# Kernel optimization log

Measured on AMD Instinct MI355X. Metric: run time of the kernel, lower is better.

## Reference

```python
import jax, jax.numpy as jnp
import numpy as np

B, IN, OUT, GD, TD, H, W, L = 16, 512, 256, 256, 256, 32, 32, 32
EPS_BN = 1e-5


def _conv2d(x, w, pad):
    return jax.lax.conv_general_dilated(
        x, w, window_strides=(1, 1), padding=[(pad, pad), (pad, pad)],
        dimension_numbers=("NCHW", "OIHW", "NCHW"))


def _up2(x):
    return jnp.repeat(jnp.repeat(x, 2, axis=2), 2, axis=3)


def _l2n(v):  # F.normalize(p=2, dim=1), eps=1e-12
    n = jnp.sqrt(jnp.sum(v * v, axis=1, keepdims=True))
    return v / jnp.maximum(n, 1e-12)


def _context(img_embs, words_embs, mask):
    i = _l2n(img_embs)            # [B, TD, P]
    wd = _l2n(words_embs)         # [B, TD, L]
    sim = jnp.einsum("bcp,bcl->bpl", i, wd)
    sim = jnp.where(mask[:, None, :], -jnp.inf, sim)
    attn = jax.nn.softmax(sim, axis=-1)
    return jnp.einsum("bpl,bcl->bcp", attn, wd)  # [B, TD, P]


def _bn(x, w, b):  # training-mode BatchNorm2d, biased variance
    m = jnp.mean(x, axis=(0, 2, 3), keepdims=True)
    v = jnp.var(x, axis=(0, 2, 3), keepdims=True)
    return (x - m) * jax.lax.rsqrt(v + EPS_BN) * w[None, :, None, None] + b[None, :, None, None]


def setup_inputs():
    key = jax.random.key(0)
    ks = jax.random.split(key, 16)
    s = 0.02
    COND = GD + TD
    return {
        "x": jax.random.normal(ks[0], (B, IN, H, W), jnp.float32),
        "global_cond": jax.random.normal(ks[1], (B, GD), jnp.float32),
        "words_embs": jax.random.normal(ks[2], (B, TD, L), jnp.float32),
        "mask": jax.random.randint(ks[3], (B, L), 0, 2).astype(bool),
        "w_img1": jax.random.normal(ks[4], (TD, IN), jnp.float32) * s,
        "w_img2": jax.random.normal(ks[5], (TD, OUT), jnp.float32) * s,
        "w_c1": jax.random.normal(ks[6], (OUT, IN, 3, 3), jnp.float32) * s,
        "w_c2": jax.random.normal(ks[7], (OUT, OUT, 3, 3), jnp.float32) * s,
        "bn1_w": jnp.ones((IN,), jnp.float32),
        "bn1_b": jnp.zeros((IN,), jnp.float32),
        "bn2_w": jnp.ones((OUT,), jnp.float32),
        "bn2_b": jnp.zeros((OUT,), jnp.float32),
        "w_g1": jax.random.normal(ks[8], (IN, COND), jnp.float32) * s,
        "b_g1": jnp.zeros((IN,), jnp.float32),
        "w_b1": jax.random.normal(ks[9], (IN, COND), jnp.float32) * s,
        "b_b1": jnp.zeros((IN,), jnp.float32),
        "w_g2": jax.random.normal(ks[10], (OUT, COND), jnp.float32) * s,
        "b_g2": jnp.zeros((OUT,), jnp.float32),
        "w_b2": jax.random.normal(ks[11], (OUT, COND), jnp.float32) * s,
        "b_b2": jnp.zeros((OUT,), jnp.float32),
        "w_sc": jax.random.normal(ks[12], (OUT, IN, 1, 1), jnp.float32) * s,
        "b_sc": jnp.zeros((OUT,), jnp.float32),
    }


def reference(x, global_cond, words_embs, mask,
              w_img1, w_img2, w_c1, w_c2,
              bn1_w, bn1_b, bn2_w, bn2_b,
              w_g1, b_g1, w_b1, b_b1,
              w_g2, b_g2, w_b2, b_b2,
              w_sc, b_sc):
    # ---- residual path, stage 1 ----
    img1 = jnp.einsum("tc,bcp->btp", w_img1, x.reshape(B, IN, H * W))
    ctx1 = _context(img1, words_embs, mask)                 # [B, TD, H*W]
    gc = jnp.broadcast_to(global_cond[:, :, None], (B, GD, H * W))
    cond1 = jnp.concatenate([gc, ctx1], axis=1)             # [B, GD+TD, H*W]
    gamma1 = jnp.einsum("oc,bcp->bop", w_g1, cond1) + b_g1[None, :, None]
    beta1 = jnp.einsum("oc,bcp->bop", w_b1, cond1) + b_b1[None, :, None]
    out = gamma1.reshape(B, IN, H, W) * _bn(x, bn1_w, bn1_b) + beta1.reshape(B, IN, H, W)
    out = jax.nn.relu(out)
    out = _up2(out)                                         # [B, IN, 2H, 2W]
    out = _conv2d(out, w_c1, 1)                             # [B, OUT, 2H, 2W]
    h2, w2 = 2 * H, 2 * W
    # ---- residual path, stage 2 ----
    img2 = jnp.einsum("tc,bcp->btp", w_img2, out.reshape(B, OUT, h2 * w2))
    ctx2 = _context(img2, words_embs, mask)                 # [B, TD, h2*w2]
    gc2 = jnp.broadcast_to(global_cond[:, :, None], (B, GD, h2 * w2))
    cond2 = jnp.concatenate([gc2, ctx2], axis=1)
    gamma2 = jnp.einsum("oc,bcp->bop", w_g2, cond2) + b_g2[None, :, None]
    beta2 = jnp.einsum("oc,bcp->bop", w_b2, cond2) + b_b2[None, :, None]
    out = gamma2.reshape(B, OUT, h2, w2) * _bn(out, bn2_w, bn2_b) + beta2.reshape(B, OUT, h2, w2)
    out = jax.nn.relu(out)
    out = _conv2d(out, w_c2, 1)
    # ---- shortcut ----
    sc = _conv2d(_up2(x), w_sc, 0) + b_sc[None, :, None, None]
    return out + sc
```

## Files before the change

### kernel.cpp

```cpp
#include <hip/hip_runtime.h>
#include <hip/hip_bf16.h>
#include <math.h>

#define NB 16
#define CIN1 512
#define COUT 256
#define GD 256
#define TD 256
#define LL 32
#define P1 1024
#define P2 4096
#define CONDC 512

typedef __attribute__((ext_vector_type(8))) short bf16x8;
typedef __attribute__((ext_vector_type(4))) float f32x4;
typedef unsigned short u16;

__device__ __forceinline__ u16 f2b(float f) {
  __hip_bfloat16 h = __float2bfloat16(f);
  return *(u16*)&h;
}
__device__ __forceinline__ float b2f(u16 v) {
  unsigned u = ((unsigned)v) << 16;
  float f;
  __builtin_memcpy(&f, &u, 4);
  return f;
}

template <bool BF>
__global__ void bn_stats_kernel(const void* xv, float* __restrict__ mean,
                                float* __restrict__ rstd, int C, int HW) {
  int c = blockIdx.x, t = threadIdx.x;
  float s = 0.f, sq = 0.f;
  for (int b = 0; b < NB; ++b) {
    size_t base = ((size_t)b * C + c) * HW;
    for (int i = t; i < HW; i += 256) {
      float v = BF ? b2f(((const u16*)xv)[base + i]) : ((const float*)xv)[base + i];
      s += v; sq += v * v;
    }
  }
  __shared__ float ss[256], sq2[256];
  ss[t] = s; sq2[t] = sq; __syncthreads();
  for (int o = 128; o > 0; o >>= 1) {
    if (t < o) { ss[t] += ss[t + o]; sq2[t] += sq2[t + o]; }
    __syncthreads();
  }
  if (t == 0) {
    float n = (float)NB * (float)HW;
    float m = ss[0] / n;
    float v = sq2[0] / n - m * m;
    mean[c] = m;
    rstd[c] = rsqrtf(v + 1e-5f);
  }
}

__global__ void bn_fin_kernel(const float* __restrict__ part, float* __restrict__ mean,
                              float* __restrict__ rstd) {
  int c = threadIdx.x;
  float s = 0.f, sq = 0.f;
  const float* ps = part + (size_t)c * 256;
  const float* pq = part + 65536 + (size_t)c * 256;
  for (int i = 0; i < 256; ++i) { s += ps[i]; sq += pq[i]; }
  float n = 16.f * 4096.f;
  float m = s / n;
  mean[c] = m;
  rstd[c] = rsqrtf(sq / n - m * m + 1e-5f);
}

__global__ void wdn_kernel(const float* __restrict__ we, float* __restrict__ wdn) {
  int b = blockIdx.x >> 5, l = blockIdx.x & 31;
  int t = threadIdx.x;
  const float* base = we + (size_t)b * TD * LL + l;
  float v[4]; float sq = 0.f;
#pragma unroll
  for (int k = 0; k < 4; ++k) { v[k] = base[(size_t)(t * 4 + k) * LL]; sq += v[k] * v[k]; }
#pragma unroll
  for (int o = 32; o > 0; o >>= 1) sq += __shfl_xor(sq, o);
  float r = 1.f / fmaxf(sqrtf(sq), 1e-12f);
  float* ob = wdn + (size_t)b * TD * LL + l;
#pragma unroll
  for (int k = 0; k < 4; ++k) ob[(size_t)(t * 4 + k) * LL] = v[k] * r;
}

__global__ __launch_bounds__(256) void attnctx_kernel(
    const u16* __restrict__ img, const float* __restrict__ wdn,
    const int* __restrict__ mask, u16* __restrict__ ctx, int P) {
  __shared__ u16 imgT[64 * 72];
  __shared__ u16 wdnT[32 * 264];
  __shared__ u16 wdnC[256 * 40];
  __shared__ u16 attnB[64 * 40];
  __shared__ float sqP[4][64];
  __shared__ float rnL[64];
  const int b = blockIdx.y, p0 = blockIdx.x * 64;
  const int tid = threadIdx.x;
  const int w = tid >> 6, lane = tid & 63;
  const int l15 = lane & 15, lg = lane >> 4;
  const u16* ib = img + (size_t)b * TD * P;
  const float* wb = wdn + (size_t)b * TD * LL;

  for (int i = tid; i < TD * LL; i += 256) {
    int t = i >> 5, l = i & 31;
    u16 v = f2b(wb[i]);
    wdnT[l * 264 + t] = v;
    wdnC[t * 40 + l] = v;
  }

  f32x4 s0 = {}, s1 = {};
  float ssq = 0.f;
  for (int q = 0; q < 4; ++q) {
#pragma unroll
    for (int i = 0; i < 16; i += 2) {
      int t = q * 64 + w * 16 + i;
      u16 h0 = ib[(size_t)t * P + p0 + lane];
      u16 h1 = ib[(size_t)(t + 1) * P + p0 + lane];
      float v0 = b2f(h0), v1 = b2f(h1);
      ssq += v0 * v0 + v1 * v1;
      unsigned pk = (unsigned)h0 | ((unsigned)h1 << 16);
      *(unsigned*)(imgT + lane * 72 + w * 16 + i) = pk;
    }
    __syncthreads();
#pragma unroll
    for (int ks = 0; ks < 2; ++ks) {
      bf16x8 a = *(const bf16x8*)(imgT + (w * 16 + l15) * 72 + ks * 32 + lg * 8);
      bf16x8 b0 = *(const bf16x8*)(wdnT + l15 * 264 + q * 64 + ks * 32 + lg * 8);
      bf16x8 b1 = *(const bf16x8*)(wdnT + (16 + l15) * 264 + q * 64 + ks * 32 + lg * 8);
      s0 = __builtin_amdgcn_mfma_f32_16x16x32_bf16(a, b0, s0, 0, 0, 0);
      s1 = __builtin_amdgcn_mfma_f32_16x16x32_bf16(a, b1, s1, 0, 0, 0);
    }
    __syncthreads();
  }
  sqP[w][lane] = ssq;
  __syncthreads();
  if (tid < 64) {
    float s = sqP[0][tid] + sqP[1][tid] + sqP[2][tid] + sqP[3][tid];
    rnL[tid] = 1.f / fmaxf(sqrtf(s), 1e-12f);
  }
  __syncthreads();
  const bool m0 = mask[b * LL + l15] != 0;
  const bool m1 = mask[b * LL + 16 + l15] != 0;
#pragma unroll
  for (int k = 0; k < 4; ++k) {
    float rn = rnL[w * 16 + lg * 4 + k];
    float v0 = m0 ? -INFINITY : s0[k] * rn;
    float v1 = m1 ? -INFINITY : s1[k] * rn;
    float mx = fmaxf(v0, v1);
#pragma unroll
    for (int o = 1; o < 16; o <<= 1) mx = fmaxf(mx, __shfl_xor(mx, o));
    float e0 = expf(v0 - mx), e1 = expf(v1 - mx);
    float sm = e0 + e1;
#pragma unroll
    for (int o = 1; o < 16; o <<= 1) sm += __shfl_xor(sm, o);
    float inv = 1.f / sm;
    int px = w * 16 + lg * 4 + k;
    attnB[px * 40 + l15] = f2b(e0 * inv);
    attnB[px * 40 + 16 + l15] = f2b(e1 * inv);
  }
  __syncthreads();
  f32x4 acc[4][4] = {};
  bf16x8 bfr[4];
#pragma unroll
  for (int pt = 0; pt < 4; ++pt)
    bfr[pt] = *(const bf16x8*)(attnB + (pt * 16 + l15) * 40 + lg * 8);
#pragma unroll
  for (int cc = 0; cc < 4; ++cc) {
    bf16x8 a = *(const bf16x8*)(wdnC + ((w * 4 + cc) * 16 + l15) * 40 + lg * 8);
#pragma unroll
    for (int pt = 0; pt < 4; ++pt)
      acc[cc][pt] = __builtin_amdgcn_mfma_f32_16x16x32_bf16(a, bfr[pt], acc[cc][pt], 0, 0, 0);
  }
#pragma unroll
  for (int cc = 0; cc < 4; ++cc) {
#pragma unroll
    for (int pt = 0; pt < 4; ++pt) {
#pragma unroll
      for (int k = 0; k < 4; ++k) {
        int c = (w * 4 + cc) * 16 + lg * 4 + k;
        ctx[((size_t)b * TD + c) * P + p0 + pt * 16 + l15] = f2b(acc[cc][pt][k]);
      }
    }
  }
}

template <bool XB, bool YB>
__global__ __launch_bounds__(256, 2) void gemm_mfma_kernel(
    const float* __restrict__ W, int ldw, int c_off,
    const void* __restrict__ Xv, const float* __restrict__ vec,
    void* __restrict__ Yv, int T, int C, int P) {
  __shared__ u16 Wl[2][128 * 44];
  __shared__ u16 Xl[2][128 * 40];
  const int b = blockIdx.z;
  const int t0 = blockIdx.y * 128, p0 = blockIdx.x * 128;
  const int tid = threadIdx.x;
  const int w = tid >> 6, lane = tid & 63;
  const int wo = w >> 1, wq = w & 1;
  const int l15 = lane & 15, lg = lane >> 4;
  const int wr = tid >> 1, wcH = tid & 1;
  const int xr = tid >> 3, xcG = tid & 7;
  const int csw = xr ^ ((xcG & 3) << 3);
  const float* wsrc = W + (size_t)(t0 + wr) * ldw + c_off + wcH * 16;
  const float* xsrc32 = XB ? nullptr : (const float*)Xv + (size_t)b * C * P + (size_t)xr * P + p0 + xcG * 16;
  const u16* xsrc16 = XB ? (const u16*)Xv + (size_t)b * C * P + (size_t)xr * P + p0 + xcG * 16 : nullptr;
  const int NK = C / 32;
  f32x4 acc[4][4] = {};
  float4 wreg[4];
  u16 xst[16];

#pragma unroll
  for (int j = 0; j < 4; ++j) wreg[j] = *(const float4*)(wsrc + j * 4);
  if (XB) {
    union { u16 u[16]; uint4 q[2]; } xu;
    xu.q[0] = *(const uint4*)(xsrc16);
    xu.q[1] = *(const uint4*)(xsrc16 + 8);
#pragma unroll
    for (int i = 0; i < 16; ++i) xst[i] = xu.u[i];
  } else {
#pragma unroll
    for (int j = 0; j < 4; ++j) {
      float4 v = *(const float4*)(xsrc32 + j * 4);
      xst[j * 4 + 0] = f2b(v.x); xst[j * 4 + 1] = f2b(v.y);
      xst[j * 4 + 2] = f2b(v.z); xst[j * 4 + 3] = f2b(v.w);
    }
  }
  {
    u16* dst = Wl[0] + wr * 44 + wcH * 16;
#pragma unroll
    for (int j = 0; j < 4; ++j)
      *(ushort4*)(dst + j * 4) = make_ushort4(f2b(wreg[j].x), f2b(wreg[j].y), f2b(wreg[j].z), f2b(wreg[j].w));
#pragma unroll
    for (int i = 0; i < 16; ++i)
      Xl[0][(xcG * 16 + i) * 40 + csw] = xst[i];
  }
  __syncthreads();

  for (int kb = 0; kb < NK; ++kb) {
    const int cur = kb & 1;
    if (kb + 1 < NK) {
      const int c0n = (kb + 1) * 32;
#pragma unroll
      for (int j = 0; j < 4; ++j) wreg[j] = *(const float4*)(wsrc + c0n + j * 4);
      if (XB) {
        union { u16 u[16]; uint4 q[2]; } xu;
        xu.q[0] = *(const uint4*)(xsrc16 + (size_t)c0n * P);
        xu.q[1] = *(const uint4*)(xsrc16 + (size_t)c0n * P + 8);
#pragma unroll
        for (int i = 0; i < 16; ++i) xst[i] = xu.u[i];
      } else {
#pragma unroll
        for (int j = 0; j < 4; ++j) {
          float4 v = *(const float4*)(xsrc32 + (size_t)c0n * P + j * 4);
          xst[j * 4 + 0] = f2b(v.x); xst[j * 4 + 1] = f2b(v.y);
          xst[j * 4 + 2] = f2b(v.z); xst[j * 4 + 3] = f2b(v.w);
        }
      }
    }
    bf16x8 a[4], bb[4];
#pragma unroll
    for (int rr = 0; rr < 4; ++rr)
      a[rr] = *(const bf16x8*)(Wl[cur] + (wo * 64 + rr * 16 + l15) * 44 + lg * 8);
#pragma unroll
    for (int ss = 0; ss < 4; ++ss)
      bb[ss] = *(const bf16x8*)(Xl[cur] + (wq * 64 + ss * 16 + l15) * 40 + ((lg ^ ss) << 3));
#pragma unroll
    for (int rr = 0; rr < 4; ++rr)
#pragma unroll
      for (int ss = 0; ss < 4; ++ss)
        acc[rr][ss] = __builtin_amdgcn_mfma_f32_16x16x32_bf16(a[rr], bb[ss], acc[rr][ss], 0, 0, 0);
    if (kb + 1 < NK) {
      const int nxt = cur ^ 1;
      u16* dst = Wl[nxt] + wr * 44 + wcH * 16;
#pragma unroll
      for (int j = 0; j < 4; ++j)
        *(ushort4*)(dst + j * 4) = make_ushort4(f2b(wreg[j].x), f2b(wreg[j].y), f2b(wreg[j].z), f2b(wreg[j].w));
#pragma unroll
      for (int i = 0; i < 16; ++i)
        Xl[nxt][(xcG * 16 + i) * 40 + csw] = xst[i];
      __syncthreads();
    }
  }
#pragma unroll
  for (int rr = 0; rr < 4; ++rr) {
    int tb = t0 + wo * 64 + rr * 16 + lg * 4;
#pragma unroll
    for (int ss = 0; ss < 4; ++ss) {
      int p = p0 + wq * 64 + ss * 16 + l15;
#pragma unroll
      for (int k = 0; k < 4; ++k) {
        int t = tb + k;
        float val = acc[rr][ss][k];
        if (vec) val += vec[(size_t)b * T + t];
        if (YB) ((u16*)Yv)[((size_t)b * T + t) * P + p] = f2b(val);
        else    ((float*)Yv)[((size_t)b * T + t) * P + p] = val;
      }
    }
  }
}

template <bool XINB>
__global__ __launch_bounds__(256, 2) void gbact_kernel(
    const float* __restrict__ Wg, const float* __restrict__ bg,
    const float* __restrict__ Wb, const float* __restrict__ bb_,
    const u16* __restrict__ ctx, const float* __restrict__ gcond,
    const void* __restrict__ xinv,
    const float* __restrict__ mean, const float* __restrict__ rstd,
    const float* __restrict__ bnw, const float* __restrict__ bnb,
    u16* __restrict__ outb, int C, int P) {
  __shared__ u16 shmem[2][16384];
  __shared__ float gvl[128], bvl[128];
  const int b = blockIdx.z, t0 = blockIdx.y * 128, p0 = blockIdx.x * 128;
  const int tid = threadIdx.x;
  const int w = tid >> 6, lane = tid & 63;
  const int wo = w >> 1, wq = w & 1;
  const int l15 = lane & 15, lg = lane >> 4;
  const int wr = tid >> 1, wcH = tid & 1;
  const int xr = tid >> 3, xcG = tid & 7;
  const int csw = xr ^ ((xcG & 3) << 3);
  const float* gsrc = Wg + (size_t)(t0 + wr) * CONDC + GD + wcH * 16;
  const float* bsrc = Wb + (size_t)(t0 + wr) * CONDC + GD + wcH * 16;
  const u16* xsrc = ctx + (size_t)b * TD * P + (size_t)xr * P + p0 + xcG * 16;
  const int NK = TD / 32;
  f32x4 accg[4][4] = {}, accb[4][4] = {};
  float4 greg[4], breg[4];
  u16 xst[16];

  {
    int t = tid & 127;
    const float* row = (tid < 128 ? Wg : Wb) + (size_t)(t0 + t) * CONDC;
    const float* gc = gcond + (size_t)b * GD;
    float s = 0.f;
    for (int c = 0; c < GD; c += 4) {
      float4 wv = *(const float4*)(row + c);
      float4 gv4 = *(const float4*)(gc + c);
      s += wv.x * gv4.x + wv.y * gv4.y + wv.z * gv4.z + wv.w * gv4.w;
    }
    s += (tid < 128 ? bg : bb_)[t0 + t];
    if (tid < 128) gvl[t] = s; else bvl[t] = s;
  }

#pragma unroll
  for (int j = 0; j < 4; ++j) {
    greg[j] = *(const float4*)(gsrc + j * 4);
    breg[j] = *(const float4*)(bsrc + j * 4);
  }
  {
    union { u16 u[16]; uint4 q[2]; } xu;
    xu.q[0] = *(const uint4*)(xsrc);
    xu.q[1] = *(const uint4*)(xsrc + 8);
#pragma unroll
    for (int i = 0; i < 16; ++i) xst[i] = xu.u[i];
  }
  {
    u16* dg = shmem[0] + wr * 44 + wcH * 16;
    u16* db = shmem[0] + 5632 + wr * 44 + wcH * 16;
    u16* xl = shmem[0] + 11264;
#pragma unroll
    for (int j = 0; j < 4; ++j) {
      *(ushort4*)(dg + j * 4) = make_ushort4(f2b(greg[j].x), f2b(greg[j].y), f2b(greg[j].z), f2b(greg[j].w));
      *(ushort4*)(db + j * 4) = make_ushort4(f2b(breg[j].x), f2b(breg[j].y), f2b(breg[j].z), f2b(breg[j].w));
    }
#pragma unroll
    for (int i = 0; i < 16; ++i)
      xl[(xcG * 16 + i) * 40 + csw] = xst[i];
  }
  __syncthreads();

  for (int kb = 0; kb < NK; ++kb) {
    const int cur = kb & 1;
    if (kb + 1 < NK) {
      const int c0n = (kb + 1) * 32;
#pragma unroll
      for (int j = 0; j < 4; ++j) {
        greg[j] = *(const float4*)(gsrc + c0n + j * 4);
        breg[j] = *(const float4*)(bsrc + c0n + j * 4);
      }
      union { u16 u[16]; uint4 q[2]; } xu;
      xu.q[0] = *(const uint4*)(xsrc + (size_t)c0n * P);
      xu.q[1] = *(const uint4*)(xsrc + (size_t)c0n * P + 8);
#pragma unroll
      for (int i = 0; i < 16; ++i) xst[i] = xu.u[i];
    }
    bf16x8 ag[4], ab[4], bb[4];
#pragma unroll
    for (int rr = 0; rr < 4; ++rr) {
      ag[rr] = *(const bf16x8*)(shmem[cur] + (wo * 64 + rr * 16 + l15) * 44 + lg * 8);
      ab[rr] = *(const bf16x8*)(shmem[cur] + 5632 + (wo * 64 + rr * 16 + l15) * 44 + lg * 8);
    }
#pragma unroll
    for (int ss = 0; ss < 4; ++ss)
      bb[ss] = *(const bf16x8*)(shmem[cur] + 11264 + (wq * 64 + ss * 16 + l15) * 40 + ((lg ^ ss) << 3));
#pragma unroll
    for (int rr = 0; rr < 4; ++rr)
#pragma unroll
      for (int ss = 0; ss < 4; ++ss) {
        accg[rr][ss] = __builtin_amdgcn_mfma_f32_16x16x32_bf16(ag[rr], bb[ss], accg[rr][ss], 0, 0, 0);
        accb[rr][ss] = __builtin_amdgcn_mfma_f32_16x16x32_bf16(ab[rr], bb[ss], accb[rr][ss], 0, 0, 0);
      }
    if (kb + 1 < NK) {
      const int nxt = cur ^ 1;
      u16* dg = shmem[nxt] + wr * 44 + wcH * 16;
      u16* db = shmem[nxt] + 5632 + wr * 44 + wcH * 16;
      u16* xl = shmem[nxt] + 11264;
#pragma unroll
      for (int j = 0; j < 4; ++j) {
        *(ushort4*)(dg + j * 4) = make_ushort4(f2b(greg[j].x), f2b(greg[j].y), f2b(greg[j].z), f2b(greg[j].w));
        *(ushort4*)(db + j * 4) = make_ushort4(f2b(breg[j].x), f2b(breg[j].y), f2b(breg[j].z), f2b(breg[j].w));
      }
#pragma unroll
      for (int i = 0; i < 16; ++i)
        xl[(xcG * 16 + i) * 40 + csw] = xst[i];
      __syncthreads();
    }
  }
  __syncthreads();
  u16* tbuf = &shmem[0][0];
#pragma unroll
  for (int rr = 0; rr < 4; ++rr) {
    float gv[4], bv[4], mm[4], rs[4], bB[4];
#pragma unroll
    for (int k = 0; k < 4; ++k) {
      int cl = wo * 64 + rr * 16 + lg * 4 + k;
      int c = t0 + cl;
      gv[k] = gvl[cl];
      bv[k] = bvl[cl];
      mm[k] = mean[c]; rs[k] = rstd[c] * bnw[c]; bB[k] = bnb[c];
    }
#pragma unroll
    for (int ss = 0; ss < 4; ++ss) {
#pragma unroll
      for (int k = 0; k < 4; ++k) {
        int cl = wo * 64 + rr * 16 + lg * 4 + k;
        int pl = wq * 64 + ss * 16 + l15;
        size_t xidx = ((size_t)b * C + t0 + cl) * P + p0 + pl;
        float xv = XINB ? b2f(((const u16*)xinv)[xidx]) : ((const float*)xinv)[xidx];
        float g = accg[rr][ss][k] + gv[k];
        float be = accb[rr][ss][k] + bv[k];
        float val = fmaxf(g * ((xv - mm[k]) * rs[k] + bB[k]) + be, 0.f);
        tbuf[pl * 136 + cl] = f2b(val);
      }
    }
  }
  __syncthreads();
  const int pr = tid >> 1, h = tid & 1;
#pragma unroll
  for (int j = 0; j < 8; ++j) {
    uint4 v = *(uint4*)(tbuf + pr * 136 + h * 64 + j * 8);
    *(uint4*)(outb + ((size_t)b * P + p0 + pr) * C + t0 + h * 64 + j * 8) = v;
  }
}

__global__ void pack2_kernel(const float* __restrict__ w1, u16* __restrict__ wp1,
                             const float* __restrict__ w2, u16* __restrict__ wp2) {
  int lin = blockIdx.x * 256 + threadIdx.x;
  const int N1 = COUT * CIN1;
  const float* w; u16* wp; int CIN;
  if (lin < N1) { w = w1; wp = wp1; CIN = CIN1; }
  else { lin -= N1; if (lin >= COUT * COUT) return; w = w2; wp = wp2; CIN = COUT; }
  int o = lin / CIN, c = lin - o * CIN;
  int c0blk = c >> 5, lg = (c >> 3) & 3, cc = c & 7;
  int ot = o >> 4, l15 = o & 15;
  int lane = lg * 16 + l15;
  size_t base = (((size_t)c0blk * (COUT >> 4) + ot) * 64 + lane) * 8 + cc;
  size_t posStride = (size_t)(CIN >> 5) * (COUT >> 4) * 512;
  const float* src = w + ((size_t)o * CIN + c) * 9;
#pragma unroll
  for (int pos = 0; pos < 9; ++pos)
    wp[pos * posStride + base] = f2b(src[pos]);
}

template <int CIN, bool UP, bool OUTB, bool STATS>
__global__ __launch_bounds__(512, 2) void conv_mfma_kernel(
    const u16* __restrict__ Wp, const u16* __restrict__ Xt,
    const float* __restrict__ scs, const float* __restrict__ scb,
    void* __restrict__ Yv, float* __restrict__ part) {
  constexpr int S = UP ? 32 : 64;
  constexpr int NC0 = CIN >> 5;
  constexpr int NCH = 6 * 66 * 8;
  __shared__ u16 Xs[2][6 * 66 * 36];
  __shared__ float stats_ls[256], stats_lsq[256];
  const int b = blockIdx.z, pxT = blockIdx.x;
  const int tid = threadIdx.x;
  const int w = tid >> 6, lane = tid & 63;
  const int wo = w >> 2, wp_ = w & 3;
  const int l15 = lane & 15, lg = lane >> 4;
  const int Y0 = pxT * 4;
  const u16* Xb = Xt + (size_t)b * S * S * CIN;
  const size_t posStride = (size_t)NC0 * 16 * 512;
  f32x4 acc[8][4] = {};
  uint2 st[7];

  if (STATS && tid < 256) { stats_ls[tid] = 0.f; stats_lsq[tid] = 0.f; }

#pragma unroll
  for (int j = 0; j < 7; ++j) {
    int i = tid + j * 512;
    if (i < NCH) {
      int r = i / 528, rem = i - r * 528, col = rem >> 3, ch = rem & 7;
      int uy = Y0 - 1 + r, ux = col - 1;
      uint2 v = make_uint2(0u, 0u);
      if (uy >= 0 && uy < 64 && ux >= 0 && ux < 64) {
        int sy = UP ? (uy >> 1) : uy, sx = UP ? (ux >> 1) : ux;
        v = *(const uint2*)(Xb + ((size_t)sy * S + sx) * CIN + ch * 4);
      }
      st[j] = v;
    }
  }
#pragma unroll
  for (int j = 0; j < 7; ++j) {
    int i = tid + j * 512;
    if (i < NCH) {
      int r = i / 528, rem = i - r * 528, col = rem >> 3, ch = rem & 7;
      *(uint2*)(&Xs[0][(r * 66 + col) * 36 + ch * 4]) = st[j];
    }
  }
  __syncthreads();

  for (int c0b = 0; c0b < NC0; ++c0b) {
    const int cur = c0b & 1;
    if (c0b + 1 < NC0) {
      const int c0n = (c0b + 1) << 5;
#pragma unroll
      for (int j = 0; j < 7; ++j) {
        int i = tid + j * 512;
        if (i < NCH) {
          int r = i / 528, rem = i - r * 528, col = rem >> 3, ch = rem & 7;
          int uy = Y0 - 1 + r, ux = col - 1;
          uint2 v = make_uint2(0u, 0u);
          if (uy >= 0 && uy < 64 && ux >= 0 && ux < 64) {
            int sy = UP ? (uy >> 1) : uy, sx = UP ? (ux >> 1) : ux;
            v = *(const uint2*)(Xb + ((size_t)sy * S + sx) * CIN + c0n + ch * 4);
          }
          st[j] = v;
        }
      }
    }
    {
      const u16* wbB = Wp + ((size_t)c0b * 16 + wo * 8) * 512 + lane * 8;
      bf16x8 aC[8], aN[8];
#pragma unroll
      for (int rr = 0; rr < 8; ++rr)
        aC[rr] = *(const bf16x8*)(wbB + rr * 512);
#pragma unroll
      for (int pos = 0; pos < 9; ++pos) {
        const int ky = pos / 3, kx = pos - ky * 3;
        if (pos < 8) {
          const u16* wbn = wbB + (size_t)(pos + 1) * posStride;
#pragma unroll
          for (int rr = 0; rr < 8; ++rr)
            aN[rr] = *(const bf16x8*)(wbn + rr * 512);
        }
        const int rowb = ((wp_ + ky) * 66 + kx) * 36 + lg * 8;
#pragma unroll
        for (int ss = 0; ss < 4; ++ss) {
          int idx = rowb + (ss * 16 + l15) * 36;
          union { uint2 q[2]; bf16x8 v; } u;
          u.q[0] = *(const uint2*)(&Xs[cur][idx]);
          u.q[1] = *(const uint2*)(&Xs[cur][idx + 4]);
#pragma unroll
          for (int rr = 0; rr < 8; ++rr)
            acc[rr][ss] = __builtin_amdgcn_mfma_f32_16x16x32_bf16(aC[rr], u.v, acc[rr][ss], 0, 0, 0);
        }
#pragma unroll
        for (int rr = 0; rr < 8; ++rr) aC[rr] = aN[rr];
      }
    }
    if (c0b + 1 < NC0) {
#pragma unroll
      for (int j = 0; j < 7; ++j) {
        int i = tid + j * 512;
        if (i < NCH) {
          int r = i / 528, rem = i - r * 528, col = rem >> 3, ch = rem & 7;
          *(uint2*)(&Xs[cur ^ 1][(r * 66 + col) * 36 + ch * 4]) = st[j];
        }
      }
      __syncthreads();
    }
  }
  const int oBase = wo * 128 + lg * 4;
  const int pxBase = pxT * 256 + wp_ * 64 + l15;
  const int y = Y0 + wp_;
#pragma unroll
  for (int rr = 0; rr < 8; ++rr) {
#pragma unroll
    for (int ss = 0; ss < 4; ++ss) {
      int px = pxBase + ss * 16;
#pragma unroll
      for (int k = 0; k < 4; ++k) {
        int o = oBase + rr * 16 + k;
        float val = acc[rr][ss][k];
        if (scs) {
          int gx = px & 63;
          val += scs[((size_t)b * COUT + o) * P1 + (y >> 1) * 32 + (gx >> 1)] + scb[o];
        }
        if (OUTB) ((u16*)Yv)[((size_t)b * COUT + o) * 4096 + px] = f2b(val);
        else      ((float*)Yv)[((size_t)b * COUT + o) * 4096 + px] = val;
      }
    }
  }
  if (STATS) {
#pragma unroll
    for (int rr = 0; rr < 8; ++rr) {
#pragma unroll
      for (int k = 0; k < 4; ++k) {
        float s = acc[rr][0][k] + acc[rr][1][k] + acc[rr][2][k] + acc[rr][3][k];
        float sq = acc[rr][0][k] * acc[rr][0][k] + acc[rr][1][k] * acc[rr][1][k] +
                   acc[rr][2][k] * acc[rr][2][k] + acc[rr][3][k] * acc[rr][3][k];
#pragma unroll
        for (int o = 1; o < 16; o <<= 1) { s += __shfl_xor(s, o); sq += __shfl_xor(sq, o); }
        if (l15 == 0) {
          int o_ = oBase + rr * 16 + k;
          atomicAdd(&stats_ls[o_], s);
          atomicAdd(&stats_lsq[o_], sq);
        }
      }
    }
    __syncthreads();
    if (tid < 256) {
      int blk = b * 16 + pxT;
      part[(size_t)tid * 256 + blk] = stats_ls[tid];
      part[65536 + (size_t)tid * 256 + blk] = stats_lsq[tid];
    }
  }
}

extern "C" void kernel_launch(void* const* d_in, const int* in_sizes, int n_in,
                              void* d_out, int out_size, void* d_ws, size_t ws_size,
                              hipStream_t stream) {
  const float* x      = (const float*)d_in[0];
  const float* gcond  = (const float*)d_in[1];
  const float* wemb   = (const float*)d_in[2];
  const int*   mask   = (const int*)d_in[3];
  const float* w_img1 = (const float*)d_in[4];
  const float* w_img2 = (const float*)d_in[5];
  const float* w_c1   = (const float*)d_in[6];
  const float* w_c2   = (const float*)d_in[7];
  const float* bn1_w  = (const float*)d_in[8];
  const float* bn1_b  = (const float*)d_in[9];
  const float* bn2_w  = (const float*)d_in[10];
  const float* bn2_b  = (const float*)d_in[11];
  const float* w_g1   = (const float*)d_in[12];
  const float* b_g1   = (const float*)d_in[13];
  const float* w_b1   = (const float*)d_in[14];
  const float* b_b1   = (const float*)d_in[15];
  const float* w_g2   = (const float*)d_in[16];
  const float* b_g2   = (const float*)d_in[17];
  const float* w_b2   = (const float*)d_in[18];
  const float* b_b2   = (const float*)d_in[19];
  const float* w_sc   = (const float*)d_in[20];
  const float* b_sc   = (const float*)d_in[21];
  float* out = (float*)d_out;
  float* ws = (float*)d_ws;

  const size_t MF = 16777216;
  float* A  = ws;
  float* Br = ws + MF;
  float* Cr = ws + 2 * MF;
  float* SM = ws + 3 * MF;
  float* wdn   = SM;
  float* mean1 = SM + 131072;
  float* rstd1 = mean1 + 512;
  float* mean2 = rstd1 + 512;
  float* rstd2 = mean2 + 256;
  float* part  = rstd2 + 256;
  float* wsp   = part + 131072;
  u16* Wp1 = (u16*)wsp;
  u16* Wp2 = (u16*)(wsp + 655360);

  u16* img1   = (u16*)A;
  u16* ctx1   = (u16*)A + 4194304;
  u16* Xt1    = (u16*)A + 8388608;
  u16* conv1o = (u16*)Cr;
  u16* img2   = (u16*)Br;
  u16* ctx2   = (u16*)A;
  u16* Xt2    = (u16*)Br;
  float* scs  = Cr;

  bn_stats_kernel<false><<<dim3(CIN1), dim3(256), 0, stream>>>(x, mean1, rstd1, CIN1, P1);
  wdn_kernel<<<dim3(NB * LL), dim3(64), 0, stream>>>(wemb, wdn);
  pack2_kernel<<<dim3((COUT * CIN1 + COUT * COUT) / 256), dim3(256), 0, stream>>>(
      w_c1, Wp1, w_c2, Wp2);
  gemm_mfma_kernel<false, true><<<dim3(P1 / 128, TD / 128, NB), dim3(256), 0, stream>>>(
      w_img1, CIN1, 0, x, nullptr, img1, TD, CIN1, P1);
  attnctx_kernel<<<dim3(P1 / 64, NB), dim3(256), 0, stream>>>(img1, wdn, mask, ctx1, P1);
  gbact_kernel<false><<<dim3(P1 / 128, CIN1 / 128, NB), dim3(256), 0, stream>>>(
      w_g1, b_g1, w_b1, b_b1, ctx1, gcond, x, mean1, rstd1, bn1_w, bn1_b, Xt1, CIN1, P1);
  conv_mfma_kernel<CIN1, true, true, true><<<dim3(16, 1, NB), dim3(512), 0, stream>>>(
      Wp1, Xt1, nullptr, nullptr, conv1o, part);

  bn_fin_kernel<<<dim3(1), dim3(256), 0, stream>>>(part, mean2, rstd2);
  gemm_mfma_kernel<true, true><<<dim3(P2 / 128, TD / 128, NB), dim3(256), 0, stream>>>(
      w_img2, COUT, 0, conv1o, nullptr, img2, TD, COUT, P2);
  attnctx_kernel<<<dim3(P2 / 64, NB), dim3(256), 0, stream>>>(img2, wdn, mask, ctx2, P2);
  gbact_kernel<true><<<dim3(P2 / 128, COUT / 128, NB), dim3(256), 0, stream>>>(
      w_g2, b_g2, w_b2, b_b2, ctx2, gcond, conv1o, mean2, rstd2, bn2_w, bn2_b, Xt2, COUT, P2);
  gemm_mfma_kernel<false, false><<<dim3(P1 / 128, COUT / 128, NB), dim3(256), 0, stream>>>(
      w_sc, CIN1, 0, x, nullptr, scs, COUT, CIN1, P1);
  conv_mfma_kernel<COUT, false, false, false><<<dim3(16, 1, NB), dim3(512), 0, stream>>>(
      Wp2, Xt2, scs, b_sc, out, nullptr);
}
```

Before: 470.0 us.

## Convert x to bf16 in BN stats pass, store shortcut in bf16, double-buffer attn

The BN-stats pass over x now also writes a bf16 copy of x. The img1 GEMM, the shortcut GEMM and the stage-1 gamma/beta kernel read that copy instead of fp32 x, which halves their input traffic. The shortcut GEMM moves earlier, writes a bf16 result into its own workspace slot, and the final conv reads it as bf16. The attention-context kernel double-buffers its image tile in shared memory so global loads for the next chunk overlap the MFMA work and one barrier per iteration is dropped. In exchange, x and the shortcut are rounded to bf16 before use, which costs some precision.

```diff
diff --git a/kernel.cpp b/kernel.cpp
--- a/kernel.cpp
+++ b/kernel.cpp
@@ -27,16 +27,17 @@
   return f;
 }
 
-template <bool BF>
-__global__ void bn_stats_kernel(const void* xv, float* __restrict__ mean,
-                                float* __restrict__ rstd, int C, int HW) {
+__global__ void bn_stats_x_kernel(const float* __restrict__ x, float* __restrict__ mean,
+                                  float* __restrict__ rstd, u16* __restrict__ xbf,
+                                  int C, int HW) {
   int c = blockIdx.x, t = threadIdx.x;
   float s = 0.f, sq = 0.f;
   for (int b = 0; b < NB; ++b) {
     size_t base = ((size_t)b * C + c) * HW;
     for (int i = t; i < HW; i += 256) {
-      float v = BF ? b2f(((const u16*)xv)[base + i]) : ((const float*)xv)[base + i];
+      float v = x[base + i];
       s += v; sq += v * v;
+      xbf[base + i] = f2b(v);
     }
   }
   __shared__ float ss[256], sq2[256];
@@ -85,7 +86,7 @@
 __global__ __launch_bounds__(256) void attnctx_kernel(
     const u16* __restrict__ img, const float* __restrict__ wdn,
     const int* __restrict__ mask, u16* __restrict__ ctx, int P) {
-  __shared__ u16 imgT[64 * 72];
+  __shared__ u16 imgT[2][64 * 72];
   __shared__ u16 wdnT[32 * 264];
   __shared__ u16 wdnC[256 * 40];
   __shared__ u16 attnB[64 * 40];
@@ -107,27 +108,48 @@
 
   f32x4 s0 = {}, s1 = {};
   float ssq = 0.f;
+  unsigned pk[8];
+#pragma unroll
+  for (int i = 0; i < 8; ++i) {
+    int t = w * 16 + 2 * i;
+    u16 h0 = ib[(size_t)t * P + p0 + lane];
+    u16 h1 = ib[(size_t)(t + 1) * P + p0 + lane];
+    float v0 = b2f(h0), v1 = b2f(h1);
+    ssq += v0 * v0 + v1 * v1;
+    pk[i] = (unsigned)h0 | ((unsigned)h1 << 16);
+  }
+#pragma unroll
+  for (int i = 0; i < 8; ++i)
+    *(unsigned*)(imgT[0] + lane * 72 + w * 16 + 2 * i) = pk[i];
+  __syncthreads();
+
   for (int q = 0; q < 4; ++q) {
-#pragma unroll
-    for (int i = 0; i < 16; i += 2) {
-      int t = q * 64 + w * 16 + i;
-      u16 h0 = ib[(size_t)t * P + p0 + lane];
-      u16 h1 = ib[(size_t)(t + 1) * P + p0 + lane];
-      float v0 = b2f(h0), v1 = b2f(h1);
-      ssq += v0 * v0 + v1 * v1;
-      unsigned pk = (unsigned)h0 | ((unsigned)h1 << 16);
-      *(unsigned*)(imgT + lane * 72 + w * 16 + i) = pk;
-    }
-    __syncthreads();
+    const int cur = q & 1;
+    if (q < 3) {
+#pragma unroll
+      for (int i = 0; i < 8; ++i) {
+        int t = (q + 1) * 64 + w * 16 + 2 * i;
+        u16 h0 = ib[(size_t)t * P + p0 + lane];
+        u16 h1 = ib[(size_t)(t + 1) * P + p0 + lane];
+        float v0 = b2f(h0), v1 = b2f(h1);
+        ssq += v0 * v0 + v1 * v1;
+        pk[i] = (unsigned)h0 | ((unsigned)h1 << 16);
+      }
+    }
 #pragma unroll
     for (int ks = 0; ks < 2; ++ks) {
-      bf16x8 a = *(const bf16x8*)(imgT + (w * 16 + l15) * 72 + ks * 32 + lg * 8);
+      bf16x8 a = *(const bf16x8*)(imgT[cur] + (w * 16 + l15) * 72 + ks * 32 + lg * 8);
       bf16x8 b0 = *(const bf16x8*)(wdnT + l15 * 264 + q * 64 + ks * 32 + lg * 8);
       bf16x8 b1 = *(const bf16x8*)(wdnT + (16 + l15) * 264 + q * 64 + ks * 32 + lg * 8);
       s0 = __builtin_amdgcn_mfma_f32_16x16x32_bf16(a, b0, s0, 0, 0, 0);
       s1 = __builtin_amdgcn_mfma_f32_16x16x32_bf16(a, b1, s1, 0, 0, 0);
     }
-    __syncthreads();
+    if (q < 3) {
+#pragma unroll
+      for (int i = 0; i < 8; ++i)
+        *(unsigned*)(imgT[cur ^ 1] + lane * 72 + w * 16 + 2 * i) = pk[i];
+      __syncthreads();
+    }
   }
   sqP[w][lane] = ssq;
   __syncthreads();
@@ -469,7 +491,7 @@
 template <int CIN, bool UP, bool OUTB, bool STATS>
 __global__ __launch_bounds__(512, 2) void conv_mfma_kernel(
     const u16* __restrict__ Wp, const u16* __restrict__ Xt,
-    const float* __restrict__ scs, const float* __restrict__ scb,
+    const u16* __restrict__ scs, const float* __restrict__ scb,
     void* __restrict__ Yv, float* __restrict__ part) {
   constexpr int S = UP ? 32 : 64;
   constexpr int NC0 = CIN >> 5;
@@ -588,7 +610,7 @@
         float val = acc[rr][ss][k];
         if (scs) {
           int gx = px & 63;
-          val += scs[((size_t)b * COUT + o) * P1 + (y >> 1) * 32 + (gx >> 1)] + scb[o];
+          val += b2f(scs[((size_t)b * COUT + o) * P1 + (y >> 1) * 32 + (gx >> 1)]) + scb[o];
         }
         if (OUTB) ((u16*)Yv)[((size_t)b * COUT + o) * 4096 + px] = f2b(val);
         else      ((float*)Yv)[((size_t)b * COUT + o) * 4096 + px] = val;
@@ -663,25 +685,28 @@
   float* wsp   = part + 131072;
   u16* Wp1 = (u16*)wsp;
   u16* Wp2 = (u16*)(wsp + 655360);
+  u16* scs = (u16*)(wsp + 655360 + 294912);
 
   u16* img1   = (u16*)A;
   u16* ctx1   = (u16*)A + 4194304;
   u16* Xt1    = (u16*)A + 8388608;
+  u16* xbf    = (u16*)A + 16777216;
   u16* conv1o = (u16*)Cr;
   u16* img2   = (u16*)Br;
   u16* ctx2   = (u16*)A;
   u16* Xt2    = (u16*)Br;
-  float* scs  = Cr;
-
-  bn_stats_kernel<false><<<dim3(CIN1), dim3(256), 0, stream>>>(x, mean1, rstd1, CIN1, P1);
+
+  bn_stats_x_kernel<<<dim3(CIN1), dim3(256), 0, stream>>>(x, mean1, rstd1, xbf, CIN1, P1);
   wdn_kernel<<<dim3(NB * LL), dim3(64), 0, stream>>>(wemb, wdn);
   pack2_kernel<<<dim3((COUT * CIN1 + COUT * COUT) / 256), dim3(256), 0, stream>>>(
       w_c1, Wp1, w_c2, Wp2);
-  gemm_mfma_kernel<false, true><<<dim3(P1 / 128, TD / 128, NB), dim3(256), 0, stream>>>(
-      w_img1, CIN1, 0, x, nullptr, img1, TD, CIN1, P1);
+  gemm_mfma_kernel<true, true><<<dim3(P1 / 128, TD / 128, NB), dim3(256), 0, stream>>>(
+      w_img1, CIN1, 0, xbf, nullptr, img1, TD, CIN1, P1);
+  gemm_mfma_kernel<true, true><<<dim3(P1 / 128, COUT / 128, NB), dim3(256), 0, stream>>>(
+      w_sc, CIN1, 0, xbf, nullptr, scs, COUT, CIN1, P1);
   attnctx_kernel<<<dim3(P1 / 64, NB), dim3(256), 0, stream>>>(img1, wdn, mask, ctx1, P1);
-  gbact_kernel<false><<<dim3(P1 / 128, CIN1 / 128, NB), dim3(256), 0, stream>>>(
-      w_g1, b_g1, w_b1, b_b1, ctx1, gcond, x, mean1, rstd1, bn1_w, bn1_b, Xt1, CIN1, P1);
+  gbact_kernel<true><<<dim3(P1 / 128, CIN1 / 128, NB), dim3(256), 0, stream>>>(
+      w_g1, b_g1, w_b1, b_b1, ctx1, gcond, xbf, mean1, rstd1, bn1_w, bn1_b, Xt1, CIN1, P1);
   conv_mfma_kernel<CIN1, true, true, true><<<dim3(16, 1, NB), dim3(512), 0, stream>>>(
       Wp1, Xt1, nullptr, nullptr, conv1o, part);
 
@@ -691,8 +716,6 @@
   attnctx_kernel<<<dim3(P2 / 64, NB), dim3(256), 0, stream>>>(img2, wdn, mask, ctx2, P2);
   gbact_kernel<true><<<dim3(P2 / 128, COUT / 128, NB), dim3(256), 0, stream>>>(
       w_g2, b_g2, w_b2, b_b2, ctx2, gcond, conv1o, mean2, rstd2, bn2_w, bn2_b, Xt2, COUT, P2);
-  gemm_mfma_kernel<false, false><<<dim3(P1 / 128, COUT / 128, NB), dim3(256), 0, stream>>>(
-      w_sc, CIN1, 0, x, nullptr, scs, COUT, CIN1, P1);
   conv_mfma_kernel<COUT, false, false, false><<<dim3(16, 1, NB), dim3(512), 0, stream>>>(
       Wp2, Xt2, scs, b_sc, out, nullptr);
 }
```

Result: no change. 461.3 us (-1.8%).
